# Kernel tuning notes

Measured on AMD Instinct MI355X. Metric: run time of the kernel, lower is better.

The kernel has to match this reference:

```python
import jax, jax.numpy as jnp
import numpy as np


def setup_inputs() -> dict:
    key = jax.random.key(0)
    k1, k2, k3, k4, k5 = jax.random.split(key, 5)
    B, S, IN, OUT = 4, 2048, 4096, 4096
    x = jax.random.normal(k1, (B, S, IN), dtype=jnp.float32)
    # int8-style quantized weight stored as int32 values in [0, 255]
    weight_q = jax.random.randint(k2, (OUT, IN), 0, 255, dtype=jnp.int32)
    weight_zero_point = jax.random.randint(k3, (OUT,), 0, 255, dtype=jnp.int32)
    weight_scale = jax.random.uniform(k4, (OUT,), dtype=jnp.float32) * 0.01 + 1e-4
    bias = jax.random.normal(k5, (OUT,), dtype=jnp.float32)
    return {"x": x, "weight_q": weight_q, "weight_zero_point": weight_zero_point,
            "weight_scale": weight_scale, "bias": bias}


def reference(x, weight_q, weight_zero_point, weight_scale, bias):
    # Decompress (dequantize) the weight: per-output-channel affine int8 quantization
    # w_fp = (w_q - zero_point) * scale   -> shape [out, in]
    w = (weight_q - weight_zero_point[:, None]).astype(jnp.float32) * weight_scale[:, None]
    # F.linear: y = x @ w.T + bias
    return jnp.einsum('bsi,oi->bso', x, w) + bias
```

## Files before the change

### kernel.cpp

```cpp
#include <hip/hip_runtime.h>
#include <hip/hip_bf16.h>
#include <stdint.h>

typedef __attribute__((ext_vector_type(4))) int i32x4;

#define K_TOT 4096
#define N_TOT 4096

__global__ __launch_bounds__(512) void prep_kernel(const float4* __restrict__ x4,
                                                   unsigned int* __restrict__ xq_dw,
                                                   float* __restrict__ s_row,
                                                   int* __restrict__ qsum_row,
                                                   const int4* __restrict__ wq,
                                                   unsigned int* __restrict__ w8,
                                                   int nqb) {
    const int wave = threadIdx.x >> 6, lane = threadIdx.x & 63;
    if ((int)blockIdx.x < nqb) {
        const long row = (long)blockIdx.x * 8 + wave;
        const float4* xr = x4 + row * (K_TOT / 4);
        float4 v[16];
        float amax = 0.f;
#pragma unroll
        for (int i = 0; i < 16; ++i) {
            v[i] = xr[lane + i * 64];
            amax = fmaxf(amax, fmaxf(fmaxf(fabsf(v[i].x), fabsf(v[i].y)),
                                     fmaxf(fabsf(v[i].z), fabsf(v[i].w))));
        }
#pragma unroll
        for (int off = 32; off; off >>= 1) amax = fmaxf(amax, __shfl_xor(amax, off));
        amax = fmaxf(amax, 1e-30f);
        const float inv = 127.0f / amax;
        int qsum = 0;
        unsigned int* out = xq_dw + row * (K_TOT / 4);
#pragma unroll
        for (int i = 0; i < 16; ++i) {
            int q0 = (int)rintf(v[i].x * inv), q1 = (int)rintf(v[i].y * inv);
            int q2 = (int)rintf(v[i].z * inv), q3 = (int)rintf(v[i].w * inv);
            qsum += q0 + q1 + q2 + q3;
            out[lane + i * 64] = (unsigned int)(q0 & 255) | ((unsigned int)(q1 & 255) << 8) |
                                 ((unsigned int)(q2 & 255) << 16) | ((unsigned int)(q3 & 255) << 24);
        }
#pragma unroll
        for (int off = 32; off; off >>= 1) qsum += __shfl_xor(qsum, off);
        if (lane == 0) { s_row[row] = amax / 127.0f; qsum_row[row] = qsum; }
    } else {
        const long o = (long)((int)blockIdx.x - nqb) * 8 + wave;
        const int4* src = wq + o * (K_TOT / 4);
        unsigned int* dst = w8 + o * (K_TOT / 4);
#pragma unroll
        for (int i = 0; i < 16; ++i) {
            int4 q = src[lane + i * 64];
            dst[lane + i * 64] =
                (unsigned int)((q.x - 128) & 255) | ((unsigned int)((q.y - 128) & 255) << 8) |
                ((unsigned int)((q.z - 128) & 255) << 16) | ((unsigned int)((q.w - 128) & 255) << 24);
        }
    }
}


template<int MH>
__device__ __forceinline__ void read_a8(i32x4 (&a)[4], const char* Ab, int wr, int fr, int kg) {
    const int sw = (fr >> 1) & 3;
#pragma unroll
    for (int mi = 0; mi < 4; ++mi) {
        const int row = wr * 128 + (MH * 4 + mi) * 16 + fr;
        a[mi] = *(const i32x4*)(Ab + row * 64 + ((kg ^ sw) << 4));
    }
}

template<int NH>
__device__ __forceinline__ void read_b8(i32x4 (&b)[2], const char* Bb, int rb, int fr, int kg) {
    const int sw = (fr >> 1) & 3;
#pragma unroll
    for (int ni = 0; ni < 2; ++ni) {
        const int row = rb + (NH * 2 + ni) * 16 + fr;
        b[ni] = *(const i32x4*)(Bb + row * 64 + ((kg ^ sw) << 4));
    }
}

template<int MH, int NH>
__device__ __forceinline__ void mfma8(i32x4 (&acc)[8][4], i32x4 (&a)[4], i32x4 (&b)[2]) {
#pragma unroll
    for (int mi = 0; mi < 4; ++mi)
#pragma unroll
        for (int ni = 0; ni < 2; ++ni)
            acc[MH * 4 + mi][NH * 2 + ni] = __builtin_amdgcn_mfma_i32_16x16x64_i8(
                a[mi], b[ni], acc[MH * 4 + mi][NH * 2 + ni], 0, 0, 0);
}

#define BAR() __builtin_amdgcn_s_barrier()
#define LGKM0() asm volatile("s_waitcnt lgkmcnt(0)" ::: "memory")
#define VMCNT2() asm volatile("s_waitcnt vmcnt(2)" ::: "memory")
#define VMCNT0() asm volatile("s_waitcnt vmcnt(0)" ::: "memory")
#define PRIO1() __builtin_amdgcn_s_setprio(1)
#define PRIO0() __builtin_amdgcn_s_setprio(0)

__launch_bounds__(512, 2)
__global__ void gemm256_i8_kernel(const char* __restrict__ Aq,
                                  const char* __restrict__ Bq,
                                  const float* __restrict__ s_row,
                                  const int* __restrict__ qsum_row,
                                  const float* __restrict__ scale,
                                  const int* __restrict__ zp,
                                  const float* __restrict__ bias,
                                  float* __restrict__ C) {
    __shared__ __align__(16) char lds[4][256 * 64];

    const int nbn = N_TOT / 256;
    int bid = blockIdx.x;
    const int nwg = gridDim.x;
    if ((nwg & 7) == 0) {
        const int cpx = nwg >> 3;
        bid = (bid & 7) * cpx + (bid >> 3);
    }
    const int bm = bid / nbn, bn = bid % nbn;

    const int tid = threadIdx.x;
    const int w = tid >> 6, lane = tid & 63;
    const int wr = w >> 2, wc = w & 3;
    const int fr = lane & 15, kg = lane >> 4;
    const int brb = (wc >> 1) * 128 + (wc & 1) * 64;

    const long a_row0 = (long)bm * 256;
    const long b_row0 = (long)bn * 256;

    i32x4 acc[8][4] = {};
    i32x4 afr[4], b0[2], b1[2];

    auto stage = [&](int t, int mat, int half) {
        const char* G = (mat == 0) ? Aq : Bq;
        const long row0 = ((mat == 0) ? a_row0 : b_row0) + half * 128;
        char* lb = &lds[(t & 1) * 2 + mat][half * 8192 + w * 1024];
        const int row = w * 16 + (lane >> 2);
        const int c = (lane & 3) ^ (((half * 128 + row) >> 1) & 3);
        const char* g = G + (row0 + row) * K_TOT + (long)t * 64 + c * 16;
        __builtin_amdgcn_global_load_lds(
            (const __attribute__((address_space(1))) void*)g,
            (__attribute__((address_space(3))) void*)lb, 16, 0, 0);
    };

    const char* Ab0 = &lds[0][0];
    const char* Bb0 = &lds[1][0];
    const char* Ab1 = &lds[2][0];
    const char* Bb1 = &lds[3][0];

    stage(0, 0, 0); stage(0, 0, 1); stage(0, 1, 0); stage(0, 1, 1);
    stage(1, 1, 0); stage(1, 1, 1);
    VMCNT2();
    BAR();

    const int NIT = K_TOT / 128;
#pragma unroll 1
    for (int it = 0; it < NIT; ++it) {
        const bool nl = (it != NIT - 1);
        const int t1 = 2 * it + 1, t2 = 2 * it + 2, t3 = 2 * it + 3;

        read_a8<0>(afr, Ab0, wr, fr, kg);
        read_b8<0>(b0, Bb0, brb, fr, kg);
        read_b8<1>(b1, Bb0, brb, fr, kg);
        stage(t1, 0, 0); stage(t1, 0, 1);
        BAR(); LGKM0();
        PRIO1(); mfma8<0, 0>(acc, afr, b0); mfma8<0, 1>(acc, afr, b1); PRIO0();
        BAR();
        read_a8<1>(afr, Ab0, wr, fr, kg);
        if (nl) { stage(t2, 1, 0); stage(t2, 1, 1); }
        BAR(); LGKM0();
        PRIO1(); mfma8<1, 1>(acc, afr, b1); mfma8<1, 0>(acc, afr, b0); PRIO0();
        if (nl) { VMCNT2(); } else { VMCNT0(); }
        BAR();
        read_a8<0>(afr, Ab1, wr, fr, kg);
        read_b8<0>(b0, Bb1, brb, fr, kg);
        read_b8<1>(b1, Bb1, brb, fr, kg);
        if (nl) { stage(t2, 0, 0); stage(t2, 0, 1); }
        BAR(); LGKM0();
        PRIO1(); mfma8<0, 0>(acc, afr, b0); mfma8<0, 1>(acc, afr, b1); PRIO0();
        BAR();
        read_a8<1>(afr, Ab1, wr, fr, kg);
        if (nl) { stage(t3, 1, 0); stage(t3, 1, 1); }
        BAR(); LGKM0();
        PRIO1(); mfma8<1, 1>(acc, afr, b1); mfma8<1, 0>(acc, afr, b0); PRIO0();
        if (nl) { VMCNT2(); }
        BAR();
    }

    float scs[4], c1s[4], bbs[4]; int cols[4];
#pragma unroll
    for (int n = 0; n < 4; ++n) {
        cols[n] = (int)b_row0 + wc * 64 + n * 16 + fr;
        scs[n] = scale[cols[n]];
        c1s[n] = (float)(128 - zp[cols[n]]);
        bbs[n] = bias[cols[n]];
    }
#pragma unroll
    for (int m = 0; m < 8; ++m) {
#pragma unroll
        for (int j = 0; j < 4; ++j) {
            const long r = a_row0 + wr * 128 + m * 16 + kg * 4 + j;
            const float sr = s_row[r];
            const float qs = (float)qsum_row[r];
#pragma unroll
            for (int n = 0; n < 4; ++n)
                C[r * N_TOT + cols[n]] = ((float)acc[m][n][j] + c1s[n] * qs) * (scs[n] * sr) + bbs[n];
        }
    }
}

__global__ void fallback_kernel(const float* __restrict__ x, const int* __restrict__ wq,
                                const int* __restrict__ zp, const float* __restrict__ sc,
                                const float* __restrict__ bs, float* __restrict__ y) {
    __shared__ float xs[32][33];
    __shared__ float ws[32][33];
    int bm = blockIdx.y, bn = blockIdx.x;
    int tid = threadIdx.x;
    int r = tid >> 5, c = tid & 31;
    float acc[4] = {0.f, 0.f, 0.f, 0.f};
    for (int k0 = 0; k0 < K_TOT; k0 += 32) {
        for (int t = tid; t < 32 * 32; t += 256) {
            int rr = t >> 5, cc = t & 31;
            xs[rr][cc] = x[(long)(bm * 32 + rr) * K_TOT + k0 + cc];
            int o = bn * 32 + rr;
            ws[rr][cc] = (float)(wq[(long)o * K_TOT + k0 + cc] - zp[o]);
        }
        __syncthreads();
#pragma unroll
        for (int kk = 0; kk < 32; ++kk) {
            float wv = ws[c][kk];
#pragma unroll
            for (int j = 0; j < 4; ++j) acc[j] += xs[r + 8 * j][kk] * wv;
        }
        __syncthreads();
    }
    int o = bn * 32 + c;
    float s = sc[o], b = bs[o];
#pragma unroll
    for (int j = 0; j < 4; ++j)
        y[(long)(bm * 32 + r + 8 * j) * N_TOT + o] = acc[j] * s + b;
}

extern "C" void kernel_launch(void* const* d_in, const int* in_sizes, int n_in,
                              void* d_out, int out_size, void* d_ws, size_t ws_size,
                              hipStream_t stream) {
    const float* x = (const float*)d_in[0];
    const int* wq = (const int*)d_in[1];
    const int* zp = (const int*)d_in[2];
    const float* sc = (const float*)d_in[3];
    const float* bs = (const float*)d_in[4];
    float* y = (float*)d_out;

    const long M = (long)in_sizes[0] / K_TOT;

    size_t xq_bytes = (size_t)M * K_TOT;
    size_t w8_bytes = (size_t)N_TOT * K_TOT;
    size_t s_bytes = (size_t)M * 4;
    size_t q_bytes = (size_t)M * 4;
    size_t need = xq_bytes + w8_bytes + s_bytes + q_bytes + 256;

    if (ws_size >= need && (M & 255) == 0) {
        char* p = (char*)d_ws;
        char* xq = p;                       p += xq_bytes;
        char* w8 = p;                       p += w8_bytes;
        float* s_row = (float*)p;           p += s_bytes;
        int* qsum_row = (int*)p;

        const int nqb = (int)(M / 8);
        const int npb = N_TOT / 8;
        prep_kernel<<<nqb + npb, 512, 0, stream>>>(
            (const float4*)x, (unsigned int*)xq, s_row, qsum_row,
            (const int4*)wq, (unsigned int*)w8, nqb);

        dim3 grid((unsigned)((M / 256) * (N_TOT / 256)));
        gemm256_i8_kernel<<<grid, 512, 0, stream>>>(
            xq, w8, s_row, qsum_row, sc, zp, bs, y);
    } else {
        dim3 grid(N_TOT / 32, (unsigned)(M / 32));
        fallback_kernel<<<grid, 256, 0, stream>>>(x, wq, zp, sc, bs, y);
    }
}
```

Before: 193.6 us.

## Load B fragments directly from global into registers, keep only A in LDS

The int8 weight operand (B) is no longer staged through LDS. Each wave now reads its B fragments straight from global memory into registers, double-buffered as even and odd k-steps. Only the activation operand A stays in LDS, which halves the shared-memory footprint, and the launch bound drops to one block per CU. The aim is to cut LDS traffic and barrier-bound B reads. In exchange, B is fetched redundantly by both wave rows, the global access pattern is only partly coalesced (64 contiguous bytes per row), and occupancy is lower.

New measurement: 263.5 us. 36.1% more time.

```diff
diff --git a/kernel.cpp b/kernel.cpp
--- a/kernel.cpp
+++ b/kernel.cpp
@@ -68,34 +68,25 @@
     }
 }
 
-template<int NH>
-__device__ __forceinline__ void read_b8(i32x4 (&b)[2], const char* Bb, int rb, int fr, int kg) {
-    const int sw = (fr >> 1) & 3;
-#pragma unroll
-    for (int ni = 0; ni < 2; ++ni) {
-        const int row = rb + (NH * 2 + ni) * 16 + fr;
-        b[ni] = *(const i32x4*)(Bb + row * 64 + ((kg ^ sw) << 4));
-    }
-}
-
-template<int MH, int NH>
-__device__ __forceinline__ void mfma8(i32x4 (&acc)[8][4], i32x4 (&a)[4], i32x4 (&b)[2]) {
+template<int MH>
+__device__ __forceinline__ void mfma16(i32x4 (&acc)[8][4], i32x4 (&a)[4], i32x4 (&b)[4]) {
+    __builtin_amdgcn_s_setprio(1);
 #pragma unroll
     for (int mi = 0; mi < 4; ++mi)
 #pragma unroll
-        for (int ni = 0; ni < 2; ++ni)
-            acc[MH * 4 + mi][NH * 2 + ni] = __builtin_amdgcn_mfma_i32_16x16x64_i8(
-                a[mi], b[ni], acc[MH * 4 + mi][NH * 2 + ni], 0, 0, 0);
+        for (int ni = 0; ni < 4; ++ni)
+            acc[MH * 4 + mi][ni] = __builtin_amdgcn_mfma_i32_16x16x64_i8(
+                a[mi], b[ni], acc[MH * 4 + mi][ni], 0, 0, 0);
+    __builtin_amdgcn_s_setprio(0);
 }
 
 #define BAR() __builtin_amdgcn_s_barrier()
 #define LGKM0() asm volatile("s_waitcnt lgkmcnt(0)" ::: "memory")
-#define VMCNT2() asm volatile("s_waitcnt vmcnt(2)" ::: "memory")
+#define VMCNT4() asm volatile("s_waitcnt vmcnt(4)" ::: "memory")
 #define VMCNT0() asm volatile("s_waitcnt vmcnt(0)" ::: "memory")
-#define PRIO1() __builtin_amdgcn_s_setprio(1)
-#define PRIO0() __builtin_amdgcn_s_setprio(0)
-
-__launch_bounds__(512, 2)
+#define FENCE() asm volatile("" ::: "memory")
+
+__launch_bounds__(512, 1)
 __global__ void gemm256_i8_kernel(const char* __restrict__ Aq,
                                   const char* __restrict__ Bq,
                                   const float* __restrict__ s_row,
@@ -104,7 +95,7 @@
                                   const int* __restrict__ zp,
                                   const float* __restrict__ bias,
                                   float* __restrict__ C) {
-    __shared__ __align__(16) char lds[4][256 * 64];
+    __shared__ __align__(16) char lds[2][256 * 64];
 
     const int nbn = N_TOT / 256;
     int bid = blockIdx.x;
@@ -125,68 +116,70 @@
     const long b_row0 = (long)bn * 256;
 
     i32x4 acc[8][4] = {};
-    i32x4 afr[4], b0[2], b1[2];
-
-    auto stage = [&](int t, int mat, int half) {
-        const char* G = (mat == 0) ? Aq : Bq;
-        const long row0 = ((mat == 0) ? a_row0 : b_row0) + half * 128;
-        char* lb = &lds[(t & 1) * 2 + mat][half * 8192 + w * 1024];
+    i32x4 afr[4], b_ev[4], b_od[4];
+
+    const char* Bg = Bq + (b_row0 + brb) * (long)K_TOT + kg * 16;
+    int boff[4];
+#pragma unroll
+    for (int q = 0; q < 4; ++q) boff[q] = (q * 16 + fr) * K_TOT;
+
+    auto loadB = [&](i32x4 (&b)[4], int t) {
+        const char* p = Bg + t * 64;
+#pragma unroll
+        for (int q = 0; q < 4; ++q) b[q] = *(const i32x4*)(p + boff[q]);
+    };
+
+    auto stage = [&](int t, int half) {
+        char* lb = &lds[t & 1][half * 8192 + w * 1024];
         const int row = w * 16 + (lane >> 2);
         const int c = (lane & 3) ^ (((half * 128 + row) >> 1) & 3);
-        const char* g = G + (row0 + row) * K_TOT + (long)t * 64 + c * 16;
+        const char* g = Aq + (a_row0 + half * 128 + row) * (long)K_TOT + (long)t * 64 + c * 16;
         __builtin_amdgcn_global_load_lds(
             (const __attribute__((address_space(1))) void*)g,
             (__attribute__((address_space(3))) void*)lb, 16, 0, 0);
     };
 
-    const char* Ab0 = &lds[0][0];
-    const char* Bb0 = &lds[1][0];
-    const char* Ab1 = &lds[2][0];
-    const char* Bb1 = &lds[3][0];
-
-    stage(0, 0, 0); stage(0, 0, 1); stage(0, 1, 0); stage(0, 1, 1);
-    stage(1, 1, 0); stage(1, 1, 1);
-    VMCNT2();
+    stage(0, 0); stage(0, 1);
+    FENCE();
+    loadB(b_ev, 0);
+    loadB(b_od, 1);
+    VMCNT4();
     BAR();
 
     const int NIT = K_TOT / 128;
 #pragma unroll 1
     for (int it = 0; it < NIT; ++it) {
         const bool nl = (it != NIT - 1);
-        const int t1 = 2 * it + 1, t2 = 2 * it + 2, t3 = 2 * it + 3;
-
-        read_a8<0>(afr, Ab0, wr, fr, kg);
-        read_b8<0>(b0, Bb0, brb, fr, kg);
-        read_b8<1>(b1, Bb0, brb, fr, kg);
-        stage(t1, 0, 0); stage(t1, 0, 1);
-        BAR(); LGKM0();
-        PRIO1(); mfma8<0, 0>(acc, afr, b0); mfma8<0, 1>(acc, afr, b1); PRIO0();
-        BAR();
-        read_a8<1>(afr, Ab0, wr, fr, kg);
-        if (nl) { stage(t2, 1, 0); stage(t2, 1, 1); }
-        BAR(); LGKM0();
-        PRIO1(); mfma8<1, 1>(acc, afr, b1); mfma8<1, 0>(acc, afr, b0); PRIO0();
-        if (nl) { VMCNT2(); } else { VMCNT0(); }
-        BAR();
-        read_a8<0>(afr, Ab1, wr, fr, kg);
-        read_b8<0>(b0, Bb1, brb, fr, kg);
-        read_b8<1>(b1, Bb1, brb, fr, kg);
-        if (nl) { stage(t2, 0, 0); stage(t2, 0, 1); }
-        BAR(); LGKM0();
-        PRIO1(); mfma8<0, 0>(acc, afr, b0); mfma8<0, 1>(acc, afr, b1); PRIO0();
-        BAR();
-        read_a8<1>(afr, Ab1, wr, fr, kg);
-        if (nl) { stage(t3, 1, 0); stage(t3, 1, 1); }
-        BAR(); LGKM0();
-        PRIO1(); mfma8<1, 1>(acc, afr, b1); mfma8<1, 0>(acc, afr, b0); PRIO0();
-        if (nl) { VMCNT2(); }
+        const int o = 2 * it + 1, e2 = 2 * it + 2, o2 = 2 * it + 3;
+        const char* Ab_e = &lds[0][0];
+        const char* Ab_o = &lds[1][0];
+
+        read_a8<0>(afr, Ab_e, wr, fr, kg);
+        stage(o, 0); stage(o, 1);
+        BAR(); LGKM0();
+        mfma16<0>(acc, afr, b_ev);
+        BAR();
+        read_a8<1>(afr, Ab_e, wr, fr, kg);
+        BAR(); LGKM0();
+        mfma16<1>(acc, afr, b_ev);
+        if (nl) { loadB(b_ev, e2); VMCNT4(); } else { VMCNT0(); }
+        BAR();
+        read_a8<0>(afr, Ab_o, wr, fr, kg);
+        if (nl) { stage(e2, 0); stage(e2, 1); }
+        BAR(); LGKM0();
+        mfma16<0>(acc, afr, b_od);
+        BAR();
+        read_a8<1>(afr, Ab_o, wr, fr, kg);
+        BAR(); LGKM0();
+        mfma16<1>(acc, afr, b_od);
+        if (nl) { loadB(b_od, o2); VMCNT4(); }
         BAR();
     }
 
     float scs[4], c1s[4], bbs[4]; int cols[4];
 #pragma unroll
     for (int n = 0; n < 4; ++n) {
-        cols[n] = (int)b_row0 + wc * 64 + n * 16 + fr;
+        cols[n] = (int)b_row0 + brb + n * 16 + fr;
         scs[n] = scale[cols[n]];
         c1s[n] = (float)(128 - zp[cols[n]]);
         bbs[n] = bias[cols[n]];
```

## Shrink int8 GEMM tile to 256x128 with 4-wave workgroups

Applied to the files above, without the earlier changes.

Replaces the 256x256 tile processed by 8 waves with a 256x128 tile processed by 4 waves. Each wave still computes a 128x64 sub-tile, and the global-to-LDS staging is rewritten so each wave issues 4 A loads and 2 B loads per k-step. LDS use per workgroup drops from 64KB to 48KB, which could allow more resident workgroups and doubles the grid size. The cost is lower A-tile reuse per workgroup, so more global and L2 traffic per unit of compute. The vmcnt wait counts were left as before even though each stage now issues a different number of loads, which could affect correctness or pipelining.

Result: slower. 202.8 us (+4.7%).

```diff
diff --git a/kernel.cpp b/kernel.cpp
--- a/kernel.cpp
+++ b/kernel.cpp
@@ -95,8 +95,8 @@
 #define PRIO1() __builtin_amdgcn_s_setprio(1)
 #define PRIO0() __builtin_amdgcn_s_setprio(0)
 
-__launch_bounds__(512, 2)
-__global__ void gemm256_i8_kernel(const char* __restrict__ Aq,
+__launch_bounds__(256, 2)
+__global__ void gemm128_i8_kernel(const char* __restrict__ Aq,
                                   const char* __restrict__ Bq,
                                   const float* __restrict__ s_row,
                                   const int* __restrict__ qsum_row,
@@ -104,9 +104,10 @@
                                   const int* __restrict__ zp,
                                   const float* __restrict__ bias,
                                   float* __restrict__ C) {
-    __shared__ __align__(16) char lds[4][256 * 64];
-
-    const int nbn = N_TOT / 256;
+    __shared__ __align__(16) char lds_a[2][256 * 64];
+    __shared__ __align__(16) char lds_b[2][128 * 64];
+
+    const int nbn = N_TOT / 128;
     int bid = blockIdx.x;
     const int nwg = gridDim.x;
     if ((nwg & 7) == 0) {
@@ -117,35 +118,44 @@
 
     const int tid = threadIdx.x;
     const int w = tid >> 6, lane = tid & 63;
-    const int wr = w >> 2, wc = w & 3;
+    const int wr = w >> 1, wc = w & 1;
     const int fr = lane & 15, kg = lane >> 4;
-    const int brb = (wc >> 1) * 128 + (wc & 1) * 64;
+    const int brb = wc * 64;
 
     const long a_row0 = (long)bm * 256;
-    const long b_row0 = (long)bn * 256;
+    const long b_row0 = (long)bn * 128;
 
     i32x4 acc[8][4] = {};
     i32x4 afr[4], b0[2], b1[2];
 
-    auto stage = [&](int t, int mat, int half) {
-        const char* G = (mat == 0) ? Aq : Bq;
-        const long row0 = ((mat == 0) ? a_row0 : b_row0) + half * 128;
-        char* lb = &lds[(t & 1) * 2 + mat][half * 8192 + w * 1024];
-        const int row = w * 16 + (lane >> 2);
-        const int c = (lane & 3) ^ (((half * 128 + row) >> 1) & 3);
-        const char* g = G + (row0 + row) * K_TOT + (long)t * 64 + c * 16;
-        __builtin_amdgcn_global_load_lds(
-            (const __attribute__((address_space(1))) void*)g,
-            (__attribute__((address_space(3))) void*)lb, 16, 0, 0);
+    auto stage_a = [&](int t) {
+#pragma unroll
+        for (int r = 0; r < 4; ++r) {
+            const int j = w * 4 + r;
+            char* lb = &lds_a[t & 1][j * 1024];
+            const int row = j * 16 + (lane >> 2);
+            const int c = (lane & 3) ^ ((row >> 1) & 3);
+            const char* g = Aq + (a_row0 + row) * (long)K_TOT + (long)t * 64 + c * 16;
+            __builtin_amdgcn_global_load_lds(
+                (const __attribute__((address_space(1))) void*)g,
+                (__attribute__((address_space(3))) void*)lb, 16, 0, 0);
+        }
     };
-
-    const char* Ab0 = &lds[0][0];
-    const char* Bb0 = &lds[1][0];
-    const char* Ab1 = &lds[2][0];
-    const char* Bb1 = &lds[3][0];
-
-    stage(0, 0, 0); stage(0, 0, 1); stage(0, 1, 0); stage(0, 1, 1);
-    stage(1, 1, 0); stage(1, 1, 1);
+    auto stage_b = [&](int t) {
+#pragma unroll
+        for (int r = 0; r < 2; ++r) {
+            const int j = w * 2 + r;
+            char* lb = &lds_b[t & 1][j * 1024];
+            const int row = j * 16 + (lane >> 2);
+            const int c = (lane & 3) ^ ((row >> 1) & 3);
+            const char* g = Bq + (b_row0 + row) * (long)K_TOT + (long)t * 64 + c * 16;
+            __builtin_amdgcn_global_load_lds(
+                (const __attribute__((address_space(1))) void*)g,
+                (__attribute__((address_space(3))) void*)lb, 16, 0, 0);
+        }
+    };
+
+    stage_a(0); stage_b(0); stage_b(1);
     VMCNT2();
     BAR();
 
@@ -153,30 +163,30 @@
 #pragma unroll 1
     for (int it = 0; it < NIT; ++it) {
         const bool nl = (it != NIT - 1);
-        const int t1 = 2 * it + 1, t2 = 2 * it + 2, t3 = 2 * it + 3;
-
-        read_a8<0>(afr, Ab0, wr, fr, kg);
-        read_b8<0>(b0, Bb0, brb, fr, kg);
-        read_b8<1>(b1, Bb0, brb, fr, kg);
-        stage(t1, 0, 0); stage(t1, 0, 1);
+        const int o = 2 * it + 1, e2 = 2 * it + 2, o2 = 2 * it + 3;
+
+        read_a8<0>(afr, lds_a[0], wr, fr, kg);
+        read_b8<0>(b0, lds_b[0], brb, fr, kg);
+        read_b8<1>(b1, lds_b[0], brb, fr, kg);
+        stage_a(o);
         BAR(); LGKM0();
         PRIO1(); mfma8<0, 0>(acc, afr, b0); mfma8<0, 1>(acc, afr, b1); PRIO0();
         BAR();
-        read_a8<1>(afr, Ab0, wr, fr, kg);
-        if (nl) { stage(t2, 1, 0); stage(t2, 1, 1); }
+        read_a8<1>(afr, lds_a[0], wr, fr, kg);
+        if (nl) stage_b(e2);
         BAR(); LGKM0();
         PRIO1(); mfma8<1, 1>(acc, afr, b1); mfma8<1, 0>(acc, afr, b0); PRIO0();
         if (nl) { VMCNT2(); } else { VMCNT0(); }
         BAR();
-        read_a8<0>(afr, Ab1, wr, fr, kg);
-        read_b8<0>(b0, Bb1, brb, fr, kg);
-        read_b8<1>(b1, Bb1, brb, fr, kg);
-        if (nl) { stage(t2, 0, 0); stage(t2, 0, 1); }
+        read_a8<0>(afr, lds_a[1], wr, fr, kg);
+        read_b8<0>(b0, lds_b[1], brb, fr, kg);
+        read_b8<1>(b1, lds_b[1], brb, fr, kg);
+        if (nl) stage_a(e2);
         BAR(); LGKM0();
         PRIO1(); mfma8<0, 0>(acc, afr, b0); mfma8<0, 1>(acc, afr, b1); PRIO0();
         BAR();
-        read_a8<1>(afr, Ab1, wr, fr, kg);
-        if (nl) { stage(t3, 1, 0); stage(t3, 1, 1); }
+        read_a8<1>(afr, lds_a[1], wr, fr, kg);
+        if (nl) stage_b(o2);
         BAR(); LGKM0();
         PRIO1(); mfma8<1, 1>(acc, afr, b1); mfma8<1, 0>(acc, afr, b0); PRIO0();
         if (nl) { VMCNT2(); }
@@ -186,7 +196,7 @@
     float scs[4], c1s[4], bbs[4]; int cols[4];
 #pragma unroll
     for (int n = 0; n < 4; ++n) {
-        cols[n] = (int)b_row0 + wc * 64 + n * 16 + fr;
+        cols[n] = (int)b_row0 + brb + n * 16 + fr;
         scs[n] = scale[cols[n]];
         c1s[n] = (float)(128 - zp[cols[n]]);
         bbs[n] = bias[cols[n]];
@@ -268,8 +278,8 @@
             (const float4*)x, (unsigned int*)xq, s_row, qsum_row,
             (const int4*)wq, (unsigned int*)w8, nqb);
 
-        dim3 grid((unsigned)((M / 256) * (N_TOT / 256)));
-        gemm256_i8_kernel<<<grid, 512, 0, stream>>>(
+        dim3 grid((unsigned)((M / 256) * (N_TOT / 128)));
+        gemm128_i8_kernel<<<grid, 256, 0, stream>>>(
             xq, w8, s_row, qsum_row, sc, zp, bs, y);
     } else {
         dim3 grid(N_TOT / 32, (unsigned)(M / 32));
```
